# Kernel tuning notes

Measured on AMD Instinct MI355X. Metric: run time of the kernel, lower is better.

The kernel has to match this reference:

```python
import math
import jax, jax.numpy as jnp
import numpy as np

NUM_HEADS = 8


def setup_inputs() -> dict:
    rng = jax.random.key(0)
    ks = jax.random.split(rng, 6)
    S, B, E = 2048, 4, 512
    scale = 1.0 / math.sqrt(E)  # xavier-ish init scale
    return {
        "query": jax.random.normal(ks[0], (S, B, E), jnp.float32),
        "key": jax.random.normal(ks[1], (S, B, E), jnp.float32),
        "value": jax.random.normal(ks[2], (S, B, E), jnp.float32),
        "attn_mask": jax.random.normal(ks[3], (B, S, S), jnp.float32),
        "in_proj_weight": jax.random.normal(ks[4], (3 * E, E), jnp.float32) * scale,
        "in_proj_bias": jnp.zeros((3 * E,), jnp.float32),
        "out_proj_weight": jax.random.normal(ks[5], (E, E), jnp.float32) * scale,
        "out_proj_bias": jnp.zeros((E,), jnp.float32),
    }


def reference(query, key, value, attn_mask, in_proj_weight, in_proj_bias,
              out_proj_weight, out_proj_bias):
    # Layout: [S, B, E] (batch_first=False)
    S, B, E = query.shape
    H = NUM_HEADS
    D = E // H
    w_q, w_k, w_v = jnp.split(in_proj_weight, 3, axis=0)  # each [E, E]
    b_q, b_k, b_v = jnp.split(in_proj_bias, 3)
    q = query @ w_q.T + b_q
    k = key @ w_k.T + b_k
    v = value @ w_v.T + b_v

    def to_heads(x):  # [S,B,E] -> [B,H,S,D]
        return x.reshape(S, B, H, D).transpose(1, 2, 0, 3)

    qh = to_heads(q) * (1.0 / math.sqrt(D))
    kh = to_heads(k)
    vh = to_heads(v)
    # full score matrix [B,H,S,S] with per-batch additive mask broadcast over heads
    scores = jnp.einsum('bhsd,bhtd->bhst', qh, kh) + attn_mask[:, None, :, :]
    attn = jax.nn.softmax(scores, axis=-1)
    out = jnp.einsum('bhst,bhtd->bhsd', attn, vh)
    out = out.transpose(2, 0, 1, 3).reshape(S, B, E)  # back to [S,B,E]
    return out @ out_proj_weight.T + out_proj_bias
```

## Files before the change

kernel.cpp:

```cpp
#include <hip/hip_runtime.h>


#define L2E 1.44269504088896340736f

typedef __attribute__((ext_vector_type(8))) __bf16 bf16x8;
typedef __attribute__((ext_vector_type(4))) float f32x4;
typedef __attribute__((ext_vector_type(16))) float f32x16;

static __device__ __forceinline__ unsigned pk2(float a, float b) {
    union { unsigned u; __bf16 h[2]; } cv;
    cv.h[0] = (__bf16)a; cv.h[1] = (__bf16)b;
    return cv.u;
}

static __device__ __forceinline__ unsigned short f2bf(float f) {
    union { unsigned short s; __bf16 h; } cv;
    cv.h = (__bf16)f;
    return cv.s;
}

__global__ __launch_bounds__(256) void qkv_kernel(
    const float* __restrict__ Xq, const float* __restrict__ Xk,
    const float* __restrict__ Xv, const float* __restrict__ W,
    const float* __restrict__ bias,
    unsigned short* __restrict__ Qp, unsigned short* __restrict__ Kp,
    unsigned short* __restrict__ Vt)
{
    __shared__ unsigned short lA[128][40];
    __shared__ unsigned short lB[128][40];

    const int z = blockIdx.z;
    const float* X  = (z == 0) ? Xq : (z == 1) ? Xk : Xv;
    const float* Wz = W + (size_t)z * 512 * 512;
    const int rb = blockIdx.y * 128;
    const int nb = blockIdx.x * 128;
    const int tid  = threadIdx.x;
    const int lane = tid & 63, wave = tid >> 6;
    const int wr = wave >> 1, wc = wave & 1;
    const int lq = lane & 15, lg = lane >> 4;

    f32x4 acc[4][4];
#pragma unroll
    for (int i = 0; i < 4; ++i)
#pragma unroll
        for (int j = 0; j < 4; ++j) acc[i][j] = (f32x4){0.f, 0.f, 0.f, 0.f};

    const int srow = tid >> 1;
    const int scol = (tid & 1) * 16;

    for (int kt = 0; kt < 16; ++kt) {
        const int k0 = kt * 32;
        if (kt) __syncthreads();
        {
            const float* g = X + (size_t)(rb + srow) * 512 + k0 + scol;
            float4 x0 = *(const float4*)(g + 0);
            float4 x1 = *(const float4*)(g + 4);
            float4 x2 = *(const float4*)(g + 8);
            float4 x3 = *(const float4*)(g + 12);
            uint4 w0, w1;
            w0.x = pk2(x0.x, x0.y); w0.y = pk2(x0.z, x0.w);
            w0.z = pk2(x1.x, x1.y); w0.w = pk2(x1.z, x1.w);
            w1.x = pk2(x2.x, x2.y); w1.y = pk2(x2.z, x2.w);
            w1.z = pk2(x3.x, x3.y); w1.w = pk2(x3.z, x3.w);
            *(uint4*)&lA[srow][scol] = w0;
            *(uint4*)&lA[srow][scol + 8] = w1;
        }
        {
            const float* g = Wz + (size_t)(nb + srow) * 512 + k0 + scol;
            float4 x0 = *(const float4*)(g + 0);
            float4 x1 = *(const float4*)(g + 4);
            float4 x2 = *(const float4*)(g + 8);
            float4 x3 = *(const float4*)(g + 12);
            uint4 w0, w1;
            w0.x = pk2(x0.x, x0.y); w0.y = pk2(x0.z, x0.w);
            w0.z = pk2(x1.x, x1.y); w0.w = pk2(x1.z, x1.w);
            w1.x = pk2(x2.x, x2.y); w1.y = pk2(x2.z, x2.w);
            w1.z = pk2(x3.x, x3.y); w1.w = pk2(x3.z, x3.w);
            *(uint4*)&lB[srow][scol] = w0;
            *(uint4*)&lB[srow][scol + 8] = w1;
        }
        __syncthreads();

        bf16x8 af[4], bf[4];
#pragma unroll
        for (int mi = 0; mi < 4; ++mi)
            af[mi] = *(const bf16x8*)&lA[wr * 64 + mi * 16 + lq][lg * 8];
#pragma unroll
        for (int ni = 0; ni < 4; ++ni)
            bf[ni] = *(const bf16x8*)&lB[wc * 64 + ni * 16 + lq][lg * 8];
#pragma unroll
        for (int mi = 0; mi < 4; ++mi)
#pragma unroll
            for (int ni = 0; ni < 4; ++ni)
                acc[mi][ni] = __builtin_amdgcn_mfma_f32_16x16x32_bf16(
                    af[mi], bf[ni], acc[mi][ni], 0, 0, 0);
    }

    const float* bz = bias + z * 512;
#pragma unroll
    for (int ni = 0; ni < 4; ++ni) {
        const int n = nb + wc * 64 + ni * 16 + lq;
        const float bv = bz[n];
        const int h = n >> 6, d = n & 63;
#pragma unroll
        for (int mi = 0; mi < 4; ++mi) {
#pragma unroll
            for (int r = 0; r < 4; ++r) {
                const int t = rb + wr * 64 + mi * 16 + lg * 4 + r;
                float v = acc[mi][ni][r] + bv;
                const int s = t >> 2, b = t & 3;
                if (z == 0) {
                    v *= 0.125f * L2E;
                    Qp[((size_t)(b * 8 + h) * 2048 + s) * 64 + d] = f2bf(v);
                } else if (z == 1) {
                    Kp[((size_t)(b * 8 + h) * 2048 + s) * 64 + d] = f2bf(v);
                } else {
                    Vt[((size_t)(b * 8 + h) * 64 + d) * 2048 + s] = f2bf(v);
                }
            }
        }
    }
}

#define SWAP32(a, b) asm("v_permlane32_swap_b32 %0, %1" : "+v"(a), "+v"(b))

#define COMPUTE(KBASE, VBASE, M) do {                                          \
    bf16x8 pf[4];                                                              \
    _Pragma("unroll")                                                          \
    for (int kblk = 0; kblk < 2; ++kblk) {                                     \
        f32x16 z;                                                              \
        _Pragma("unroll")                                                      \
        for (int g = 0; g < 4; ++g) {                                          \
            z[4*g+0] = M[kblk][g].x * L2E;                                     \
            z[4*g+1] = M[kblk][g].y * L2E;                                     \
            z[4*g+2] = M[kblk][g].z * L2E;                                     \
            z[4*g+3] = M[kblk][g].w * L2E;                                     \
        }                                                                      \
        __builtin_amdgcn_s_setprio(1);                                         \
        _Pragma("unroll")                                                      \
        for (int s = 0; s < 4; ++s) {                                          \
            bf16x8 kf = *(const bf16x8*)((KBASE) + fof[kblk][s]);              \
            z = __builtin_amdgcn_mfma_f32_32x32x16_bf16(kf, qf[s], z, 0,0,0);  \
        }                                                                      \
        __builtin_amdgcn_s_setprio(0);                                         \
        float p[16];                                                           \
        _Pragma("unroll")                                                      \
        for (int i = 0; i < 16; ++i) p[i] = exp2f(z[i]);                       \
        lsum += (((p[0]+p[1])+(p[2]+p[3])) + ((p[4]+p[5])+(p[6]+p[7])))        \
              + (((p[8]+p[9])+(p[10]+p[11])) + ((p[12]+p[13])+(p[14]+p[15]))); \
        unsigned a0 = pk2(p[0], p[1]),   b0 = pk2(p[4], p[5]);                 \
        unsigned a1 = pk2(p[2], p[3]),   b1 = pk2(p[6], p[7]);                 \
        SWAP32(a0, b0); SWAP32(a1, b1);                                        \
        union { unsigned w[4]; bf16x8 v; } u0;                                 \
        u0.w[0] = a0; u0.w[1] = a1; u0.w[2] = b0; u0.w[3] = b1;                \
        pf[kblk*2] = u0.v;                                                     \
        unsigned c0 = pk2(p[8], p[9]),   d0 = pk2(p[12], p[13]);               \
        unsigned c1 = pk2(p[10], p[11]), d1 = pk2(p[14], p[15]);               \
        SWAP32(c0, d0); SWAP32(c1, d1);                                        \
        union { unsigned w[4]; bf16x8 v; } u1;                                 \
        u1.w[0] = c0; u1.w[1] = c1; u1.w[2] = d0; u1.w[3] = d1;                \
        pf[kblk*2+1] = u1.v;                                                   \
    }                                                                          \
    __builtin_amdgcn_s_setprio(1);                                             \
    _Pragma("unroll")                                                          \
    for (int s = 0; s < 4; ++s) {                                              \
        bf16x8 vf0 = *(const bf16x8*)((VBASE) + fof[0][s]);                    \
        o0 = __builtin_amdgcn_mfma_f32_32x32x16_bf16(vf0, pf[s], o0, 0,0,0);   \
        bf16x8 vf1 = *(const bf16x8*)((VBASE) + fof[1][s]);                    \
        o1 = __builtin_amdgcn_mfma_f32_32x32x16_bf16(vf1, pf[s], o1, 0,0,0);   \
    }                                                                          \
    __builtin_amdgcn_s_setprio(0);                                             \
} while (0)

__global__ __launch_bounds__(256, 2) void attn_kernel(
    const unsigned short* __restrict__ Qp, const unsigned short* __restrict__ Kp,
    const unsigned short* __restrict__ Vt, const float* __restrict__ mask,
    unsigned short* __restrict__ AO)
{
    __shared__ unsigned short lK[2][64][64];
    __shared__ unsigned short lV[2][64][64];

    const int bh = blockIdx.y;
    const int b = bh >> 3, h = bh & 7;
    const int qb = blockIdx.x * 128;
    const int tid  = threadIdx.x;
    const int lane = tid & 63, wave = tid >> 6;
    const int lc = lane & 31, hi = lane >> 5;

    const int qg = qb + wave * 32 + lc;

    bf16x8 qf[4];
    {
        const unsigned short* qp = Qp + ((size_t)bh * 2048 + qg) * 64 + hi * 8;
#pragma unroll
        for (int s = 0; s < 4; ++s)
            qf[s] = *(const bf16x8*)(qp + s * 16);
    }

    f32x16 o0, o1;
#pragma unroll
    for (int i = 0; i < 16; ++i) { o0[i] = 0.f; o1[i] = 0.f; }
    float lsum = 0.f;

    int fof[2][4];
#pragma unroll
    for (int blk = 0; blk < 2; ++blk)
#pragma unroll
        for (int s = 0; s < 4; ++s)
            fof[blk][s] = (blk * 32 + lc) * 128 +
                          ((((s << 1) | hi) ^ (lane & 7)) * 16);

    const int srow = tid >> 2;
    const int scu  = (tid & 3) * 2;
    const int su0  = (scu    ) ^ (srow & 7);
    const int su1  = (scu + 1) ^ (srow & 7);
    const unsigned short* gK = Kp + (size_t)bh * 2048 * 64 + (size_t)srow * 64 + scu * 8;
    const unsigned short* gV = Vt + (size_t)bh * 64 * 2048 + (size_t)srow * 2048 + scu * 8;
    const float* mbase = mask + ((size_t)b * 2048 + qg) * 2048 + hi * 4;

    float4 mA[2][4], mB[2][4];

    {
        uint4 ka = *(const uint4*)(gK);
        uint4 kc = *(const uint4*)(gK + 8);
        uint4 va = *(const uint4*)(gV);
        uint4 vc = *(const uint4*)(gV + 8);
#pragma unroll
        for (int kblk = 0; kblk < 2; ++kblk)
#pragma unroll
            for (int g = 0; g < 4; ++g)
                mA[kblk][g] = *(const float4*)(mbase + kblk * 32 + g * 8);
        *(uint4*)&lK[0][srow][su0 * 8] = ka;
        *(uint4*)&lK[0][srow][su1 * 8] = kc;
        *(uint4*)&lV[0][srow][su0 * 8] = va;
        *(uint4*)&lV[0][srow][su1 * 8] = vc;
    }
    __syncthreads();

    const unsigned short* pgK = gK + 64 * 64;
    const unsigned short* pgV = gV + 64;
    const float* pm = mbase + 64;

    for (int kb2 = 0; kb2 < 16; ++kb2) {
        {
            uint4 ka = *(const uint4*)(pgK);
            uint4 kc = *(const uint4*)(pgK + 8);
            uint4 va = *(const uint4*)(pgV);
            uint4 vc = *(const uint4*)(pgV + 8);
#pragma unroll
            for (int kblk = 0; kblk < 2; ++kblk)
#pragma unroll
                for (int g = 0; g < 4; ++g)
                    mB[kblk][g] = *(const float4*)(pm + kblk * 32 + g * 8);
            pgK += 64 * 64; pgV += 64; pm += 64;

            COMPUTE((const char*)&lK[0][0][0], (const char*)&lV[0][0][0], mA);

            *(uint4*)&lK[1][srow][su0 * 8] = ka;
            *(uint4*)&lK[1][srow][su1 * 8] = kc;
            *(uint4*)&lV[1][srow][su0 * 8] = va;
            *(uint4*)&lV[1][srow][su1 * 8] = vc;
            __syncthreads();
        }
        {
            uint4 ka, kc, va, vc;
            if (kb2 < 15) {
                ka = *(const uint4*)(pgK);
                kc = *(const uint4*)(pgK + 8);
                va = *(const uint4*)(pgV);
                vc = *(const uint4*)(pgV + 8);
#pragma unroll
                for (int kblk = 0; kblk < 2; ++kblk)
#pragma unroll
                    for (int g = 0; g < 4; ++g)
                        mA[kblk][g] = *(const float4*)(pm + kblk * 32 + g * 8);
                pgK += 64 * 64; pgV += 64; pm += 64;
            }

            COMPUTE((const char*)&lK[1][0][0], (const char*)&lV[1][0][0], mB);

            if (kb2 < 15) {
                *(uint4*)&lK[0][srow][su0 * 8] = ka;
                *(uint4*)&lK[0][srow][su1 * 8] = kc;
                *(uint4*)&lV[0][srow][su0 * 8] = va;
                *(uint4*)&lV[0][srow][su1 * 8] = vc;
                __syncthreads();
            }
        }
    }

    lsum += __shfl_xor(lsum, 32);
    const float inv = 1.0f / lsum;

    unsigned short* ao = AO + ((size_t)qg * 4 + b) * 512 + h * 64;
#pragma unroll
    for (int g = 0; g < 4; ++g) {
        const int d0 = g * 8 + hi * 4;
        *(uint2*)(ao + d0) =
            make_uint2(pk2(o0[4*g+0] * inv, o0[4*g+1] * inv),
                       pk2(o0[4*g+2] * inv, o0[4*g+3] * inv));
        *(uint2*)(ao + 32 + d0) =
            make_uint2(pk2(o1[4*g+0] * inv, o1[4*g+1] * inv),
                       pk2(o1[4*g+2] * inv, o1[4*g+3] * inv));
    }
}

__global__ __launch_bounds__(256) void oproj_kernel(
    const unsigned short* __restrict__ A, const float* __restrict__ W,
    const float* __restrict__ bias, float* __restrict__ out)
{
    __shared__ unsigned short lA[128][40];
    __shared__ unsigned short lB[128][40];

    const int rb = blockIdx.y * 128;
    const int nb = blockIdx.x * 128;
    const int tid  = threadIdx.x;
    const int lane = tid & 63, wave = tid >> 6;
    const int wr = wave >> 1, wc = wave & 1;
    const int lq = lane & 15, lg = lane >> 4;

    f32x4 acc[4][4];
#pragma unroll
    for (int i = 0; i < 4; ++i)
#pragma unroll
        for (int j = 0; j < 4; ++j) acc[i][j] = (f32x4){0.f, 0.f, 0.f, 0.f};

    const int srow = tid >> 1;
    const int scol = (tid & 1) * 16;

    for (int kt = 0; kt < 16; ++kt) {
        const int k0 = kt * 32;
        if (kt) __syncthreads();
        {
            const unsigned short* g = A + (size_t)(rb + srow) * 512 + k0 + scol;
            *(uint4*)&lA[srow][scol]     = *(const uint4*)g;
            *(uint4*)&lA[srow][scol + 8] = *(const uint4*)(g + 8);
        }
        {
            const float* g = W + (size_t)(nb + srow) * 512 + k0 + scol;
            float4 x0 = *(const float4*)(g + 0);
            float4 x1 = *(const float4*)(g + 4);
            float4 x2 = *(const float4*)(g + 8);
            float4 x3 = *(const float4*)(g + 12);
            uint4 w0, w1;
            w0.x = pk2(x0.x, x0.y); w0.y = pk2(x0.z, x0.w);
            w0.z = pk2(x1.x, x1.y); w0.w = pk2(x1.z, x1.w);
            w1.x = pk2(x2.x, x2.y); w1.y = pk2(x2.z, x2.w);
            w1.z = pk2(x3.x, x3.y); w1.w = pk2(x3.z, x3.w);
            *(uint4*)&lB[srow][scol] = w0;
            *(uint4*)&lB[srow][scol + 8] = w1;
        }
        __syncthreads();

        bf16x8 af[4], bfr[4];
#pragma unroll
        for (int mi = 0; mi < 4; ++mi)
            af[mi] = *(const bf16x8*)&lA[wr * 64 + mi * 16 + lq][lg * 8];
#pragma unroll
        for (int ni = 0; ni < 4; ++ni)
            bfr[ni] = *(const bf16x8*)&lB[wc * 64 + ni * 16 + lq][lg * 8];
#pragma unroll
        for (int mi = 0; mi < 4; ++mi)
#pragma unroll
            for (int ni = 0; ni < 4; ++ni)
                acc[mi][ni] = __builtin_amdgcn_mfma_f32_16x16x32_bf16(
                    af[mi], bfr[ni], acc[mi][ni], 0, 0, 0);
    }

#pragma unroll
    for (int ni = 0; ni < 4; ++ni) {
        const int n = nb + wc * 64 + ni * 16 + lq;
        const float bv = bias[n];
#pragma unroll
        for (int mi = 0; mi < 4; ++mi) {
#pragma unroll
            for (int r = 0; r < 4; ++r) {
                const int t = rb + wr * 64 + mi * 16 + lg * 4 + r;
                out[(size_t)t * 512 + n] = acc[mi][ni][r] + bv;
            }
        }
    }
}

extern "C" void kernel_launch(void* const* d_in, const int* in_sizes, int n_in,
                              void* d_out, int out_size, void* d_ws, size_t ws_size,
                              hipStream_t stream)
{
    (void)in_sizes; (void)n_in; (void)out_size; (void)ws_size;
    const float* query = (const float*)d_in[0];
    const float* key   = (const float*)d_in[1];
    const float* value = (const float*)d_in[2];
    const float* mask  = (const float*)d_in[3];
    const float* w_in  = (const float*)d_in[4];
    const float* b_in  = (const float*)d_in[5];
    const float* w_out = (const float*)d_in[6];
    const float* b_out = (const float*)d_in[7];
    float* out = (float*)d_out;

    char* ws = (char*)d_ws;
    unsigned short* Qp = (unsigned short*)(ws);
    unsigned short* Kp = (unsigned short*)(ws + (size_t)8 * 1024 * 1024);
    unsigned short* Vt = (unsigned short*)(ws + (size_t)16 * 1024 * 1024);
    unsigned short* AO = (unsigned short*)(ws + (size_t)24 * 1024 * 1024);

    qkv_kernel<<<dim3(4, 64, 3), 256, 0, stream>>>(query, key, value, w_in, b_in,
                                                   Qp, Kp, Vt);
    attn_kernel<<<dim3(16, 32), 256, 0, stream>>>(Qp, Kp, Vt, mask, AO);
    oproj_kernel<<<dim3(4, 64), 256, 0, stream>>>(AO, w_out, b_out, out);
}
```

Before: 157.6 us.

## Stage mask tiles through shared memory with coalesced loads, single-buffer K/V

The attention mask was previously loaded by each lane directly from global memory in a strided pattern (each lane reads its own query row, float4 chunks 8 apart). It is now loaded cooperatively, 16 threads per row of 64 contiguous floats, pre-scaled by log2(e), and stored into a padded LDS tile. Each lane then reads its mask values from LDS. K/V double buffering is replaced by a single buffer with an extra barrier per iteration, which frees LDS for the mask tile. This adds LDS traffic and synchronization and may reduce overlap.

```diff
diff --git a/kernel.cpp b/kernel.cpp
--- a/kernel.cpp
+++ b/kernel.cpp
@@ -124,22 +124,20 @@
 
 #define SWAP32(a, b) asm("v_permlane32_swap_b32 %0, %1" : "+v"(a), "+v"(b))
 
-#define COMPUTE(KBASE, VBASE, M) do {                                          \
+#define COMPUTE() do {                                                         \
     bf16x8 pf[4];                                                              \
     _Pragma("unroll")                                                          \
     for (int kblk = 0; kblk < 2; ++kblk) {                                     \
         f32x16 z;                                                              \
         _Pragma("unroll")                                                      \
-        for (int g = 0; g < 4; ++g) {                                          \
-            z[4*g+0] = M[kblk][g].x * L2E;                                     \
-            z[4*g+1] = M[kblk][g].y * L2E;                                     \
-            z[4*g+2] = M[kblk][g].z * L2E;                                     \
-            z[4*g+3] = M[kblk][g].w * L2E;                                     \
-        }                                                                      \
+        for (int g = 0; g < 4; ++g)                                            \
+            _Pragma("unroll")                                                  \
+            for (int j = 0; j < 4; ++j)                                        \
+                z[4*g+j] = lM[qrow][kblk * 32 + g * 8 + hi4 + j];              \
         __builtin_amdgcn_s_setprio(1);                                         \
         _Pragma("unroll")                                                      \
         for (int s = 0; s < 4; ++s) {                                          \
-            bf16x8 kf = *(const bf16x8*)((KBASE) + fof[kblk][s]);              \
+            bf16x8 kf = *(const bf16x8*)(lKc + fof[kblk][s]);                  \
             z = __builtin_amdgcn_mfma_f32_32x32x16_bf16(kf, qf[s], z, 0,0,0);  \
         }                                                                      \
         __builtin_amdgcn_s_setprio(0);                                         \
@@ -164,9 +162,9 @@
     __builtin_amdgcn_s_setprio(1);                                             \
     _Pragma("unroll")                                                          \
     for (int s = 0; s < 4; ++s) {                                              \
-        bf16x8 vf0 = *(const bf16x8*)((VBASE) + fof[0][s]);                    \
+        bf16x8 vf0 = *(const bf16x8*)(lVc + fof[0][s]);                        \
         o0 = __builtin_amdgcn_mfma_f32_32x32x16_bf16(vf0, pf[s], o0, 0,0,0);   \
-        bf16x8 vf1 = *(const bf16x8*)((VBASE) + fof[1][s]);                    \
+        bf16x8 vf1 = *(const bf16x8*)(lVc + fof[1][s]);                        \
         o1 = __builtin_amdgcn_mfma_f32_32x32x16_bf16(vf1, pf[s], o1, 0,0,0);   \
     }                                                                          \
     __builtin_amdgcn_s_setprio(0);                                             \
@@ -177,8 +175,9 @@
     const unsigned short* __restrict__ Vt, const float* __restrict__ mask,
     unsigned short* __restrict__ AO)
 {
-    __shared__ unsigned short lK[2][64][64];
-    __shared__ unsigned short lV[2][64][64];
+    __shared__ unsigned short lK[64][64];
+    __shared__ unsigned short lV[64][64];
+    __shared__ float lM[128][65];
 
     const int bh = blockIdx.y;
     const int b = bh >> 3, h = bh & 7;
@@ -186,8 +185,12 @@
     const int tid  = threadIdx.x;
     const int lane = tid & 63, wave = tid >> 6;
     const int lc = lane & 31, hi = lane >> 5;
-
-    const int qg = qb + wave * 32 + lc;
+    const int hi4 = hi * 4;
+    const int qrow = wave * 32 + lc;
+    const int qg = qb + qrow;
+
+    const char* lKc = (const char*)&lK[0][0];
+    const char* lVc = (const char*)&lV[0][0];
 
     bf16x8 qf[4];
     {
@@ -216,76 +219,62 @@
     const int su1  = (scu + 1) ^ (srow & 7);
     const unsigned short* gK = Kp + (size_t)bh * 2048 * 64 + (size_t)srow * 64 + scu * 8;
     const unsigned short* gV = Vt + (size_t)bh * 64 * 2048 + (size_t)srow * 2048 + scu * 8;
-    const float* mbase = mask + ((size_t)b * 2048 + qg) * 2048 + hi * 4;
-
-    float4 mA[2][4], mB[2][4];
-
-    {
-        uint4 ka = *(const uint4*)(gK);
-        uint4 kc = *(const uint4*)(gK + 8);
-        uint4 va = *(const uint4*)(gV);
-        uint4 vc = *(const uint4*)(gV + 8);
-#pragma unroll
-        for (int kblk = 0; kblk < 2; ++kblk)
-#pragma unroll
-            for (int g = 0; g < 4; ++g)
-                mA[kblk][g] = *(const float4*)(mbase + kblk * 32 + g * 8);
-        *(uint4*)&lK[0][srow][su0 * 8] = ka;
-        *(uint4*)&lK[0][srow][su1 * 8] = kc;
-        *(uint4*)&lV[0][srow][su0 * 8] = va;
-        *(uint4*)&lV[0][srow][su1 * 8] = vc;
+
+    const int mq = tid >> 4;
+    const int mk = (tid & 15) * 4;
+    const float* gM = mask + ((size_t)b * 2048 + qb + mq) * 2048 + mk;
+
+    uint4 ka, kc, va, vc;
+    float4 mf[8];
+
+    ka = *(const uint4*)(gK);
+    kc = *(const uint4*)(gK + 8);
+    va = *(const uint4*)(gV);
+    vc = *(const uint4*)(gV + 8);
+#pragma unroll
+    for (int j = 0; j < 8; ++j)
+        mf[j] = *(const float4*)(gM + (size_t)j * 16 * 2048);
+    *(uint4*)&lK[srow][su0 * 8] = ka;
+    *(uint4*)&lK[srow][su1 * 8] = kc;
+    *(uint4*)&lV[srow][su0 * 8] = va;
+    *(uint4*)&lV[srow][su1 * 8] = vc;
+#pragma unroll
+    for (int j = 0; j < 8; ++j) {
+        lM[mq + j * 16][mk + 0] = mf[j].x * L2E;
+        lM[mq + j * 16][mk + 1] = mf[j].y * L2E;
+        lM[mq + j * 16][mk + 2] = mf[j].z * L2E;
+        lM[mq + j * 16][mk + 3] = mf[j].w * L2E;
     }
     __syncthreads();
 
-    const unsigned short* pgK = gK + 64 * 64;
-    const unsigned short* pgV = gV + 64;
-    const float* pm = mbase + 64;
-
-    for (int kb2 = 0; kb2 < 16; ++kb2) {
-        {
-            uint4 ka = *(const uint4*)(pgK);
-            uint4 kc = *(const uint4*)(pgK + 8);
-            uint4 va = *(const uint4*)(pgV);
-            uint4 vc = *(const uint4*)(pgV + 8);
-#pragma unroll
-            for (int kblk = 0; kblk < 2; ++kblk)
-#pragma unroll
-                for (int g = 0; g < 4; ++g)
-                    mB[kblk][g] = *(const float4*)(pm + kblk * 32 + g * 8);
-            pgK += 64 * 64; pgV += 64; pm += 64;
-
-            COMPUTE((const char*)&lK[0][0][0], (const char*)&lV[0][0][0], mA);
-
-            *(uint4*)&lK[1][srow][su0 * 8] = ka;
-            *(uint4*)&lK[1][srow][su1 * 8] = kc;
-            *(uint4*)&lV[1][srow][su0 * 8] = va;
-            *(uint4*)&lV[1][srow][su1 * 8] = vc;
+    for (int kb = 0; kb < 32; ++kb) {
+        if (kb < 31) {
+            const size_t kv = (size_t)(kb + 1) * 64;
+            ka = *(const uint4*)(gK + kv * 64);
+            kc = *(const uint4*)(gK + kv * 64 + 8);
+            va = *(const uint4*)(gV + kv);
+            vc = *(const uint4*)(gV + kv + 8);
+#pragma unroll
+            for (int j = 0; j < 8; ++j)
+                mf[j] = *(const float4*)(gM + (size_t)j * 16 * 2048 + kv);
+        }
+
+        COMPUTE();
+
+        __syncthreads();
+        if (kb < 31) {
+            *(uint4*)&lK[srow][su0 * 8] = ka;
+            *(uint4*)&lK[srow][su1 * 8] = kc;
+            *(uint4*)&lV[srow][su0 * 8] = va;
+            *(uint4*)&lV[srow][su1 * 8] = vc;
+#pragma unroll
+            for (int j = 0; j < 8; ++j) {
+                lM[mq + j * 16][mk + 0] = mf[j].x * L2E;
+                lM[mq + j * 16][mk + 1] = mf[j].y * L2E;
+                lM[mq + j * 16][mk + 2] = mf[j].z * L2E;
+                lM[mq + j * 16][mk + 3] = mf[j].w * L2E;
+            }
             __syncthreads();
-        }
-        {
-            uint4 ka, kc, va, vc;
-            if (kb2 < 15) {
-                ka = *(const uint4*)(pgK);
-                kc = *(const uint4*)(pgK + 8);
-                va = *(const uint4*)(pgV);
-                vc = *(const uint4*)(pgV + 8);
-#pragma unroll
-                for (int kblk = 0; kblk < 2; ++kblk)
-#pragma unroll
-                    for (int g = 0; g < 4; ++g)
-                        mA[kblk][g] = *(const float4*)(pm + kblk * 32 + g * 8);
-                pgK += 64 * 64; pgV += 64; pm += 64;
-            }
-
-            COMPUTE((const char*)&lK[1][0][0], (const char*)&lV[1][0][0], mB);
-
-            if (kb2 < 15) {
-                *(uint4*)&lK[0][srow][su0 * 8] = ka;
-                *(uint4*)&lK[0][srow][su1 * 8] = kc;
-                *(uint4*)&lV[0][srow][su0 * 8] = va;
-                *(uint4*)&lV[0][srow][su1 * 8] = vc;
-                __syncthreads();
-            }
         }
     }
 
@@ -295,7 +284,7 @@
     unsigned short* ao = AO + ((size_t)qg * 4 + b) * 512 + h * 64;
 #pragma unroll
     for (int g = 0; g < 4; ++g) {
-        const int d0 = g * 8 + hi * 4;
+        const int d0 = g * 8 + hi4;
         *(uint2*)(ao + d0) =
             make_uint2(pk2(o0[4*g+0] * inv, o0[4*g+1] * inv),
                        pk2(o0[4*g+2] * inv, o0[4*g+3] * inv));
```

Measured after the change: 163.6 us. 3.8% more time.

## Process two heads per attention block with 64 queries each and swizzled block order

Applied to the files above, without the earlier changes.

Each attention block now covers 64 query rows for two adjacent heads (two waves per head) instead of 128 query rows for a single head. The two heads share the same per-batch mask rows, so a block's mask traffic is shared across heads. The grid is flattened and remapped so that neighbouring blocks cover different head pairs on the same query tile, which is meant to improve L2 reuse of the large fp32 mask. In exchange, K/V shared memory doubles and each thread issues twice as many K/V global loads per step, which adds register and LDS pressure.

```diff
diff --git a/kernel.cpp b/kernel.cpp
--- a/kernel.cpp
+++ b/kernel.cpp
@@ -124,7 +124,7 @@
 
 #define SWAP32(a, b) asm("v_permlane32_swap_b32 %0, %1" : "+v"(a), "+v"(b))
 
-#define COMPUTE(KBASE, VBASE, M) do {                                          \
+#define COMPUTE(KC, VC, M) do {                                                \
     bf16x8 pf[4];                                                              \
     _Pragma("unroll")                                                          \
     for (int kblk = 0; kblk < 2; ++kblk) {                                     \
@@ -139,7 +139,7 @@
         __builtin_amdgcn_s_setprio(1);                                         \
         _Pragma("unroll")                                                      \
         for (int s = 0; s < 4; ++s) {                                          \
-            bf16x8 kf = *(const bf16x8*)((KBASE) + fof[kblk][s]);              \
+            bf16x8 kf = *(const bf16x8*)((KC) + fof[kblk][s]);                 \
             z = __builtin_amdgcn_mfma_f32_32x32x16_bf16(kf, qf[s], z, 0,0,0);  \
         }                                                                      \
         __builtin_amdgcn_s_setprio(0);                                         \
@@ -164,12 +164,36 @@
     __builtin_amdgcn_s_setprio(1);                                             \
     _Pragma("unroll")                                                          \
     for (int s = 0; s < 4; ++s) {                                              \
-        bf16x8 vf0 = *(const bf16x8*)((VBASE) + fof[0][s]);                    \
+        bf16x8 vf0 = *(const bf16x8*)((VC) + fof[0][s]);                       \
         o0 = __builtin_amdgcn_mfma_f32_32x32x16_bf16(vf0, pf[s], o0, 0,0,0);   \
-        bf16x8 vf1 = *(const bf16x8*)((VBASE) + fof[1][s]);                    \
+        bf16x8 vf1 = *(const bf16x8*)((VC) + fof[1][s]);                       \
         o1 = __builtin_amdgcn_mfma_f32_32x32x16_bf16(vf1, pf[s], o1, 0,0,0);   \
     }                                                                          \
     __builtin_amdgcn_s_setprio(0);                                             \
+} while (0)
+
+#define LOADNEXT(MDST) do {                                                    \
+    ka0 = *(const uint4*)(pgK0); kc0 = *(const uint4*)(pgK0 + 8);              \
+    ka1 = *(const uint4*)(pgK1); kc1 = *(const uint4*)(pgK1 + 8);              \
+    va0 = *(const uint4*)(pgV0); vc0 = *(const uint4*)(pgV0 + 8);              \
+    va1 = *(const uint4*)(pgV1); vc1 = *(const uint4*)(pgV1 + 8);              \
+    _Pragma("unroll")                                                          \
+    for (int kblk = 0; kblk < 2; ++kblk)                                       \
+        _Pragma("unroll")                                                      \
+        for (int g = 0; g < 4; ++g)                                            \
+            MDST[kblk][g] = *(const float4*)(pm + kblk * 32 + g * 8);          \
+    pgK0 += 4096; pgK1 += 4096; pgV0 += 64; pgV1 += 64; pm += 64;              \
+} while (0)
+
+#define STORE(BUF) do {                                                        \
+    *(uint4*)&lK[BUF][0][srow][su0 * 8] = ka0;                                 \
+    *(uint4*)&lK[BUF][0][srow][su1 * 8] = kc0;                                 \
+    *(uint4*)&lK[BUF][1][srow][su0 * 8] = ka1;                                 \
+    *(uint4*)&lK[BUF][1][srow][su1 * 8] = kc1;                                 \
+    *(uint4*)&lV[BUF][0][srow][su0 * 8] = va0;                                 \
+    *(uint4*)&lV[BUF][0][srow][su1 * 8] = vc0;                                 \
+    *(uint4*)&lV[BUF][1][srow][su0 * 8] = va1;                                 \
+    *(uint4*)&lV[BUF][1][srow][su1 * 8] = vc1;                                 \
 } while (0)
 
 __global__ __launch_bounds__(256, 2) void attn_kernel(
@@ -177,17 +201,21 @@
     const unsigned short* __restrict__ Vt, const float* __restrict__ mask,
     unsigned short* __restrict__ AO)
 {
-    __shared__ unsigned short lK[2][64][64];
-    __shared__ unsigned short lV[2][64][64];
-
-    const int bh = blockIdx.y;
-    const int b = bh >> 3, h = bh & 7;
-    const int qb = blockIdx.x * 128;
+    __shared__ unsigned short lK[2][2][64][64];
+    __shared__ unsigned short lV[2][2][64][64];
+
+    const int g0 = blockIdx.x;
+    const int pr = (g0 & 7) | ((g0 >> 8) << 3);
+    const int qt = (g0 >> 3) & 31;
+    const int b  = pr >> 2;
+    const int h0 = (pr & 3) << 1;
+
     const int tid  = threadIdx.x;
     const int lane = tid & 63, wave = tid >> 6;
     const int lc = lane & 31, hi = lane >> 5;
-
-    const int qg = qb + wave * 32 + lc;
+    const int hw = wave >> 1;
+    const int qg = qt * 64 + (wave & 1) * 32 + lc;
+    const int bh = b * 8 + h0 + hw;
 
     bf16x8 qf[4];
     {
@@ -209,81 +237,41 @@
         for (int s = 0; s < 4; ++s)
             fof[blk][s] = (blk * 32 + lc) * 128 +
                           ((((s << 1) | hi) ^ (lane & 7)) * 16);
+
+    const char* lK0c = (const char*)&lK[0][hw][0][0];
+    const char* lK1c = (const char*)&lK[1][hw][0][0];
+    const char* lV0c = (const char*)&lV[0][hw][0][0];
+    const char* lV1c = (const char*)&lV[1][hw][0][0];
 
     const int srow = tid >> 2;
     const int scu  = (tid & 3) * 2;
     const int su0  = (scu    ) ^ (srow & 7);
     const int su1  = (scu + 1) ^ (srow & 7);
-    const unsigned short* gK = Kp + (size_t)bh * 2048 * 64 + (size_t)srow * 64 + scu * 8;
-    const unsigned short* gV = Vt + (size_t)bh * 64 * 2048 + (size_t)srow * 2048 + scu * 8;
-    const float* mbase = mask + ((size_t)b * 2048 + qg) * 2048 + hi * 4;
-
+    const unsigned short* pgK0 = Kp + (size_t)(b*8+h0  ) * 2048 * 64 + (size_t)srow * 64   + scu * 8;
+    const unsigned short* pgK1 = Kp + (size_t)(b*8+h0+1) * 2048 * 64 + (size_t)srow * 64   + scu * 8;
+    const unsigned short* pgV0 = Vt + (size_t)(b*8+h0  ) * 64 * 2048 + (size_t)srow * 2048 + scu * 8;
+    const unsigned short* pgV1 = Vt + (size_t)(b*8+h0+1) * 64 * 2048 + (size_t)srow * 2048 + scu * 8;
+    const float* pm = mask + ((size_t)b * 2048 + qg) * 2048 + hi * 4;
+
+    uint4 ka0, kc0, ka1, kc1, va0, vc0, va1, vc1;
     float4 mA[2][4], mB[2][4];
 
-    {
-        uint4 ka = *(const uint4*)(gK);
-        uint4 kc = *(const uint4*)(gK + 8);
-        uint4 va = *(const uint4*)(gV);
-        uint4 vc = *(const uint4*)(gV + 8);
-#pragma unroll
-        for (int kblk = 0; kblk < 2; ++kblk)
-#pragma unroll
-            for (int g = 0; g < 4; ++g)
-                mA[kblk][g] = *(const float4*)(mbase + kblk * 32 + g * 8);
-        *(uint4*)&lK[0][srow][su0 * 8] = ka;
-        *(uint4*)&lK[0][srow][su1 * 8] = kc;
-        *(uint4*)&lV[0][srow][su0 * 8] = va;
-        *(uint4*)&lV[0][srow][su1 * 8] = vc;
-    }
+    LOADNEXT(mA);
+    STORE(0);
     __syncthreads();
 
-    const unsigned short* pgK = gK + 64 * 64;
-    const unsigned short* pgV = gV + 64;
-    const float* pm = mbase + 64;
-
     for (int kb2 = 0; kb2 < 16; ++kb2) {
         {
-            uint4 ka = *(const uint4*)(pgK);
-            uint4 kc = *(const uint4*)(pgK + 8);
-            uint4 va = *(const uint4*)(pgV);
-            uint4 vc = *(const uint4*)(pgV + 8);
-#pragma unroll
-            for (int kblk = 0; kblk < 2; ++kblk)
-#pragma unroll
-                for (int g = 0; g < 4; ++g)
-                    mB[kblk][g] = *(const float4*)(pm + kblk * 32 + g * 8);
-            pgK += 64 * 64; pgV += 64; pm += 64;
-
-            COMPUTE((const char*)&lK[0][0][0], (const char*)&lV[0][0][0], mA);
-
-            *(uint4*)&lK[1][srow][su0 * 8] = ka;
-            *(uint4*)&lK[1][srow][su1 * 8] = kc;
-            *(uint4*)&lV[1][srow][su0 * 8] = va;
-            *(uint4*)&lV[1][srow][su1 * 8] = vc;
+            LOADNEXT(mB);
+            COMPUTE(lK0c, lV0c, mA);
+            STORE(1);
             __syncthreads();
         }
         {
-            uint4 ka, kc, va, vc;
+            if (kb2 < 15) LOADNEXT(mA);
+            COMPUTE(lK1c, lV1c, mB);
             if (kb2 < 15) {
-                ka = *(const uint4*)(pgK);
-                kc = *(const uint4*)(pgK + 8);
-                va = *(const uint4*)(pgV);
-                vc = *(const uint4*)(pgV + 8);
-#pragma unroll
-                for (int kblk = 0; kblk < 2; ++kblk)
-#pragma unroll
-                    for (int g = 0; g < 4; ++g)
-                        mA[kblk][g] = *(const float4*)(pm + kblk * 32 + g * 8);
-                pgK += 64 * 64; pgV += 64; pm += 64;
-            }
-
-            COMPUTE((const char*)&lK[1][0][0], (const char*)&lV[1][0][0], mB);
-
-            if (kb2 < 15) {
-                *(uint4*)&lK[0][srow][su0 * 8] = ka;
-                *(uint4*)&lK[0][srow][su1 * 8] = kc;
-                *(uint4*)&lV[0][srow][su0 * 8] = va;
-                *(uint4*)&lV[0][srow][su1 * 8] = vc;
+                STORE(0);
                 __syncthreads();
             }
         }
@@ -292,7 +280,7 @@
     lsum += __shfl_xor(lsum, 32);
     const float inv = 1.0f / lsum;
 
-    unsigned short* ao = AO + ((size_t)qg * 4 + b) * 512 + h * 64;
+    unsigned short* ao = AO + ((size_t)qg * 4 + b) * 512 + (h0 + hw) * 64;
 #pragma unroll
     for (int g = 0; g < 4; ++g) {
         const int d0 = g * 8 + hi * 4;
@@ -405,6 +393,6 @@
 
     qkv_kernel<<<dim3(4, 64, 3), 256, 0, stream>>>(query, key, value, w_in, b_in,
                                                    Qp, Kp, Vt);
-    attn_kernel<<<dim3(16, 32), 256, 0, stream>>>(Qp, Kp, Vt, mask, AO);
+    attn_kernel<<<dim3(512), 256, 0, stream>>>(Qp, Kp, Vt, mask, AO);
     oproj_kernel<<<dim3(4, 64), 256, 0, stream>>>(AO, w_out, b_out, out);
 }
```

Result: slower. 169.6 us (+7.6%).
